# Optimization experiments

Measured on AMD Instinct MI355X. Metric: run time of the kernel, lower is better.

Reference implementation:

```python
import jax, jax.numpy as jnp
import numpy as np

S, B, H, L = 256, 256, 1024, 3  # seq_len, batch, hidden(=input), num_layers


def setup_inputs() -> dict:
    key = jax.random.key(0)
    k1, k2, k3 = jax.random.split(key, 3)
    scale = 1.0 / np.sqrt(H)
    return {
        "x": jax.random.normal(k1, (S, B, H), dtype=jnp.float32),
        "h_0": jnp.zeros((L, B, H), dtype=jnp.float32),
        "W_ih": jax.random.normal(k2, (L, H, H), dtype=jnp.float32) * scale,
        "W_hh": jax.random.normal(k3, (L, H, H), dtype=jnp.float32) * scale,
        "b_ih": jnp.zeros((L, H), dtype=jnp.float32),
        "b_hh": jnp.zeros((L, H), dtype=jnp.float32),
    }


def reference(x, h_0, W_ih, W_hh, b_ih, b_hh):
    L_ = W_ih.shape[0]

    def step(h_prev, x_t):
        # h_prev: [L, B, H], x_t: [B, H]
        inp = x_t
        hs = []
        for l in range(L_):
            h_l = jnp.tanh(inp @ W_ih[l].T + b_ih[l] + h_prev[l] @ W_hh[l].T + b_hh[l])
            hs.append(h_l)
            inp = h_l
        h_next = jnp.stack(hs, axis=0)
        return h_next, hs[-1]

    h_N, y = jax.lax.scan(step, h_0, x)
    return y, h_N
```

## Files before the change

### kernel.cpp

```cpp
#include <hip/hip_runtime.h>
#include <math.h>


#define S_LEN  256
#define BATCH  256
#define HID    1024
#define NLAY   3
#define RING   4
#define COLS   32
#define ROWS   128
#define GROUP  32
#define TOTAL_WG     192
#define THREADS      256

typedef _Float16 v8h __attribute__((ext_vector_type(8)));
typedef float    v4f __attribute__((ext_vector_type(4)));

#define MFMA16(a, b, c) __builtin_amdgcn_mfma_f32_16x16x32_f16((a), (b), (c), 0, 0, 0)

#define FLAG(l, t, rb) (((l) * S_LEN + (t)) * 2 + (rb))

__device__ __forceinline__ void spin_wait(int* p, int target) {
  while (__hip_atomic_load(p, __ATOMIC_RELAXED, __HIP_MEMORY_SCOPE_AGENT) < target) {
    __builtin_amdgcn_s_sleep(1);
  }
}

__global__ void rnn_pre(const float* __restrict__ x,
                        const float* __restrict__ h0,
                        _Float16* __restrict__ hring,
                        _Float16* __restrict__ x16,
                        int* __restrict__ done,
                        int convert_x) {
  const size_t idx = (size_t)blockIdx.x * blockDim.x + threadIdx.x;
  if (idx < NLAY * S_LEN * 2) done[idx] = 0;
  if (idx < (size_t)NLAY * BATCH * HID) {
    const int l   = (int)(idx / (BATCH * HID));
    const int off = (int)(idx - (size_t)l * (BATCH * HID));
    hring[(size_t)(l * RING + (RING - 1)) * BATCH * HID + off] = (_Float16)h0[idx];
  }
  if (convert_x) {
    const size_t base = idx * 8;
    if (base < (size_t)S_LEN * BATCH * HID) {
      v4f f0 = *(const v4f*)(x + base);
      v4f f1 = *(const v4f*)(x + base + 4);
      v8h v;
#pragma unroll
      for (int j = 0; j < 4; ++j) {
        v[j]     = (_Float16)f0[j];
        v[j + 4] = (_Float16)f1[j];
      }
      *(v8h*)(x16 + base) = v;
    }
  }
}

__global__ __launch_bounds__(THREADS, 1) void rnn_main(
    const float* __restrict__ x,
    const _Float16* __restrict__ x16,
    const float* __restrict__ W_ih, const float* __restrict__ W_hh,
    const float* __restrict__ b_ih, const float* __restrict__ b_hh,
    float* __restrict__ out,
    _Float16* __restrict__ hring, int* __restrict__ done) {
  __shared__ _Float16 WB[64][2][64][8];

  const int tid  = threadIdx.x;
  const int lane = tid & 63;
  const int wave = tid >> 6;
  const int wg   = blockIdx.x;
  const int l    = wg >> 6;
  const int sub  = wg & 63;
  const int rb   = sub >> 5;
  const int cb   = sub & 31;

  for (int i = tid; i < 64 * 2 * 64; i += THREADS) {
    const int kc = i >> 7;
    const int ct = (i >> 6) & 1;
    const int ln = i & 63;
    const int c    = ct * 16 + (ln & 15);
    const int k0   = kc * 32 + ((ln >> 4) << 3);
    const int gcol = cb * COLS + c;
    const float* src = (k0 < HID)
        ? (W_ih + (size_t)l * HID * HID + (size_t)gcol * HID + k0)
        : (W_hh + (size_t)l * HID * HID + (size_t)gcol * HID + (k0 - HID));
    v8h w;
#pragma unroll
    for (int j = 0; j < 8; ++j) w[j] = (_Float16)src[j];
    *(v8h*)(&WB[kc][ct][ln][0]) = w;
  }

  const int   c0    = cb * COLS + (lane & 15);
  const float bias0 = b_ih[l * HID + c0]      + b_hh[l * HID + c0];
  const float bias1 = b_ih[l * HID + c0 + 16] + b_hh[l * HID + c0 + 16];
  __syncthreads();

  const int rowbase = rb * ROWS + wave * 32;
  const int r0      = rowbase + (lane & 15);
  const int kfrag   = (lane >> 4) << 3;

  for (int t = 0; t < S_LEN; ++t) {
    v4f acc[2][2];
#pragma unroll
    for (int a = 0; a < 2; ++a)
#pragma unroll
      for (int b = 0; b < 2; ++b) acc[a][b] = (v4f){0.f, 0.f, 0.f, 0.f};

    if (l == 0) {
      if (x16) {
        const _Float16* a0p = x16 + (size_t)t * BATCH * HID + (size_t)r0 * HID + kfrag;
        const _Float16* a1p = a0p + (size_t)16 * HID;
#pragma unroll 8
        for (int kc = 0; kc < 32; ++kc) {
          v8h a0 = *(const v8h*)(a0p + kc * 32);
          v8h a1 = *(const v8h*)(a1p + kc * 32);
          v8h b0 = *(const v8h*)(&WB[kc][0][lane][0]);
          v8h b1 = *(const v8h*)(&WB[kc][1][lane][0]);
          acc[0][0] = MFMA16(a0, b0, acc[0][0]);
          acc[0][1] = MFMA16(a0, b1, acc[0][1]);
          acc[1][0] = MFMA16(a1, b0, acc[1][0]);
          acc[1][1] = MFMA16(a1, b1, acc[1][1]);
        }
      } else {
        const float* a0p = x + (size_t)t * BATCH * HID + (size_t)r0 * HID + kfrag;
        const float* a1p = a0p + (size_t)16 * HID;
#pragma unroll 4
        for (int kc = 0; kc < 32; ++kc) {
          v4f f0 = *(const v4f*)(a0p + kc * 32);
          v4f f1 = *(const v4f*)(a0p + kc * 32 + 4);
          v4f g0 = *(const v4f*)(a1p + kc * 32);
          v4f g1 = *(const v4f*)(a1p + kc * 32 + 4);
          v8h a0, a1;
#pragma unroll
          for (int j = 0; j < 4; ++j) {
            a0[j]     = (_Float16)f0[j];
            a0[j + 4] = (_Float16)f1[j];
            a1[j]     = (_Float16)g0[j];
            a1[j + 4] = (_Float16)g1[j];
          }
          v8h b0 = *(const v8h*)(&WB[kc][0][lane][0]);
          v8h b1 = *(const v8h*)(&WB[kc][1][lane][0]);
          acc[0][0] = MFMA16(a0, b0, acc[0][0]);
          acc[0][1] = MFMA16(a0, b1, acc[0][1]);
          acc[1][0] = MFMA16(a1, b0, acc[1][0]);
          acc[1][1] = MFMA16(a1, b1, acc[1][1]);
        }
      }
    }

    if (tid == 0) {
      if (t > 0)                      spin_wait(&done[FLAG(l, t - 1, rb)], GROUP);
      if (l < NLAY - 1 && t >= RING)  spin_wait(&done[FLAG(l + 1, t - RING, rb)], GROUP);
    }
    __syncthreads();
    __builtin_amdgcn_fence(__ATOMIC_ACQUIRE, "agent");

    {
      const _Float16* base = hring + (size_t)(l * RING + ((t + RING - 1) & (RING - 1))) * BATCH * HID;
      const _Float16* a0p  = base + (size_t)r0 * HID + kfrag;
      const _Float16* a1p  = a0p + (size_t)16 * HID;
#pragma unroll 8
      for (int kc = 0; kc < 32; ++kc) {
        v8h a0 = *(const v8h*)(a0p + kc * 32);
        v8h a1 = *(const v8h*)(a1p + kc * 32);
        v8h b0 = *(const v8h*)(&WB[kc + 32][0][lane][0]);
        v8h b1 = *(const v8h*)(&WB[kc + 32][1][lane][0]);
        acc[0][0] = MFMA16(a0, b0, acc[0][0]);
        acc[0][1] = MFMA16(a0, b1, acc[0][1]);
        acc[1][0] = MFMA16(a1, b0, acc[1][0]);
        acc[1][1] = MFMA16(a1, b1, acc[1][1]);
      }
    }

    if (l > 0) {
      if (tid == 0) spin_wait(&done[FLAG(l - 1, t, rb)], GROUP);
      __syncthreads();
      __builtin_amdgcn_fence(__ATOMIC_ACQUIRE, "agent");

      const _Float16* base = hring + (size_t)((l - 1) * RING + (t & (RING - 1))) * BATCH * HID;
      const _Float16* a0p  = base + (size_t)r0 * HID + kfrag;
      const _Float16* a1p  = a0p + (size_t)16 * HID;
#pragma unroll 8
      for (int kc = 0; kc < 32; ++kc) {
        v8h a0 = *(const v8h*)(a0p + kc * 32);
        v8h a1 = *(const v8h*)(a1p + kc * 32);
        v8h b0 = *(const v8h*)(&WB[kc][0][lane][0]);
        v8h b1 = *(const v8h*)(&WB[kc][1][lane][0]);
        acc[0][0] = MFMA16(a0, b0, acc[0][0]);
        acc[0][1] = MFMA16(a0, b1, acc[0][1]);
        acc[1][0] = MFMA16(a1, b0, acc[1][0]);
        acc[1][1] = MFMA16(a1, b1, acc[1][1]);
      }
    }

    _Float16* hout = hring + (size_t)(l * RING + (t & (RING - 1))) * BATCH * HID;
    float*    yout = out + (size_t)t * BATCH * HID;
    float*    hN   = out + (size_t)S_LEN * BATCH * HID + (size_t)l * BATCH * HID;
    const int qrow = (lane >> 4) << 2;
    const int ccol = lane & 15;
#pragma unroll
    for (int rt = 0; rt < 2; ++rt) {
#pragma unroll
      for (int ct = 0; ct < 2; ++ct) {
        const float bb   = (ct == 0) ? bias0 : bias1;
        const int   colg = cb * COLS + ct * 16 + ccol;
#pragma unroll
        for (int i = 0; i < 4; ++i) {
          const int rowg = rowbase + rt * 16 + qrow + i;
          const float hv = tanhf(acc[rt][ct][i] + bb);
          hout[(size_t)rowg * HID + colg] = (_Float16)hv;
          if (l == NLAY - 1)  yout[(size_t)rowg * HID + colg] = hv;
          if (t == S_LEN - 1) hN[(size_t)rowg * HID + colg]   = hv;
        }
      }
    }

    __syncthreads();
    if (tid == 0) {
      __hip_atomic_fetch_add(&done[FLAG(l, t, rb)], 1, __ATOMIC_RELEASE, __HIP_MEMORY_SCOPE_AGENT);
    }
  }
}

extern "C" void kernel_launch(void* const* d_in, const int* in_sizes, int n_in,
                              void* d_out, int out_size, void* d_ws, size_t ws_size,
                              hipStream_t stream) {
  (void)in_sizes; (void)n_in; (void)out_size;
  const float* x    = (const float*)d_in[0];
  const float* h0   = (const float*)d_in[1];
  const float* W_ih = (const float*)d_in[2];
  const float* W_hh = (const float*)d_in[3];
  const float* b_ih = (const float*)d_in[4];
  const float* b_hh = (const float*)d_in[5];
  float* out = (float*)d_out;

  int*      done  = (int*)d_ws;
  _Float16* hring = (_Float16*)((char*)d_ws + 8192);

  const size_t ring_bytes = (size_t)NLAY * RING * BATCH * HID * sizeof(_Float16);
  const size_t x16_off    = 8192 + ring_bytes;
  const size_t x16_bytes  = (size_t)S_LEN * BATCH * HID * sizeof(_Float16);
  const int    use_x16    = (ws_size >= x16_off + x16_bytes) ? 1 : 0;
  _Float16*    x16        = use_x16 ? (_Float16*)((char*)d_ws + x16_off) : (_Float16*)0;

  const int pre_elems  = use_x16 ? (S_LEN * BATCH * HID / 8) : (NLAY * BATCH * HID);
  const int pre_blocks = (pre_elems + THREADS - 1) / THREADS;
  rnn_pre<<<pre_blocks, THREADS, 0, stream>>>(x, h0, hring, x16, done, use_x16);
  rnn_main<<<TOTAL_WG, THREADS, 0, stream>>>(x, x16, W_ih, W_hh, b_ih, b_hh, out, hring, done);
}
```

Baseline: 8.737 ms.

## Use per-wave spin waits, 8 waves per block, deeper ring, fast tanh

```diff
diff --git a/kernel.cpp b/kernel.cpp
--- a/kernel.cpp
+++ b/kernel.cpp
@@ -6,12 +6,12 @@
 #define BATCH  256
 #define HID    1024
 #define NLAY   3
-#define RING   4
+#define RING   8
 #define COLS   32
 #define ROWS   128
 #define GROUP  32
 #define TOTAL_WG     192
-#define THREADS      256
+#define THREADS      512
 
 typedef _Float16 v8h __attribute__((ext_vector_type(8)));
 typedef float    v4f __attribute__((ext_vector_type(4)));
@@ -20,10 +20,15 @@
 
 #define FLAG(l, t, rb) (((l) * S_LEN + (t)) * 2 + (rb))
 
-__device__ __forceinline__ void spin_wait(int* p, int target) {
+__device__ __forceinline__ void wave_wait(int* p, int target) {
   while (__hip_atomic_load(p, __ATOMIC_RELAXED, __HIP_MEMORY_SCOPE_AGENT) < target) {
     __builtin_amdgcn_s_sleep(1);
   }
+}
+
+__device__ __forceinline__ float tanh_fast(float x) {
+  const float e = __expf(2.0f * x);
+  return 1.0f - 2.0f * __builtin_amdgcn_rcpf(e + 1.0f);
 }
 
 __global__ void rnn_pre(const float* __restrict__ x,
@@ -94,101 +99,75 @@
   const float bias1 = b_ih[l * HID + c0 + 16] + b_hh[l * HID + c0 + 16];
   __syncthreads();
 
-  const int rowbase = rb * ROWS + wave * 32;
+  const int rowbase = rb * ROWS + wave * 16;
   const int r0      = rowbase + (lane & 15);
   const int kfrag   = (lane >> 4) << 3;
 
   for (int t = 0; t < S_LEN; ++t) {
-    v4f acc[2][2];
-#pragma unroll
-    for (int a = 0; a < 2; ++a)
-#pragma unroll
-      for (int b = 0; b < 2; ++b) acc[a][b] = (v4f){0.f, 0.f, 0.f, 0.f};
+    v4f acc[2];
+    acc[0] = (v4f){0.f, 0.f, 0.f, 0.f};
+    acc[1] = (v4f){0.f, 0.f, 0.f, 0.f};
 
     if (l == 0) {
       if (x16) {
-        const _Float16* a0p = x16 + (size_t)t * BATCH * HID + (size_t)r0 * HID + kfrag;
-        const _Float16* a1p = a0p + (size_t)16 * HID;
+        const _Float16* ap = x16 + (size_t)t * BATCH * HID + (size_t)r0 * HID + kfrag;
 #pragma unroll 8
         for (int kc = 0; kc < 32; ++kc) {
-          v8h a0 = *(const v8h*)(a0p + kc * 32);
-          v8h a1 = *(const v8h*)(a1p + kc * 32);
+          v8h a  = *(const v8h*)(ap + kc * 32);
           v8h b0 = *(const v8h*)(&WB[kc][0][lane][0]);
           v8h b1 = *(const v8h*)(&WB[kc][1][lane][0]);
-          acc[0][0] = MFMA16(a0, b0, acc[0][0]);
-          acc[0][1] = MFMA16(a0, b1, acc[0][1]);
-          acc[1][0] = MFMA16(a1, b0, acc[1][0]);
-          acc[1][1] = MFMA16(a1, b1, acc[1][1]);
+          acc[0] = MFMA16(a, b0, acc[0]);
+          acc[1] = MFMA16(a, b1, acc[1]);
         }
       } else {
-        const float* a0p = x + (size_t)t * BATCH * HID + (size_t)r0 * HID + kfrag;
-        const float* a1p = a0p + (size_t)16 * HID;
+        const float* ap = x + (size_t)t * BATCH * HID + (size_t)r0 * HID + kfrag;
 #pragma unroll 4
         for (int kc = 0; kc < 32; ++kc) {
-          v4f f0 = *(const v4f*)(a0p + kc * 32);
-          v4f f1 = *(const v4f*)(a0p + kc * 32 + 4);
-          v4f g0 = *(const v4f*)(a1p + kc * 32);
-          v4f g1 = *(const v4f*)(a1p + kc * 32 + 4);
-          v8h a0, a1;
+          v4f f0 = *(const v4f*)(ap + kc * 32);
+          v4f f1 = *(const v4f*)(ap + kc * 32 + 4);
+          v8h a;
 #pragma unroll
           for (int j = 0; j < 4; ++j) {
-            a0[j]     = (_Float16)f0[j];
-            a0[j + 4] = (_Float16)f1[j];
-            a1[j]     = (_Float16)g0[j];
-            a1[j + 4] = (_Float16)g1[j];
+            a[j]     = (_Float16)f0[j];
+            a[j + 4] = (_Float16)f1[j];
           }
           v8h b0 = *(const v8h*)(&WB[kc][0][lane][0]);
           v8h b1 = *(const v8h*)(&WB[kc][1][lane][0]);
-          acc[0][0] = MFMA16(a0, b0, acc[0][0]);
-          acc[0][1] = MFMA16(a0, b1, acc[0][1]);
-          acc[1][0] = MFMA16(a1, b0, acc[1][0]);
-          acc[1][1] = MFMA16(a1, b1, acc[1][1]);
+          acc[0] = MFMA16(a, b0, acc[0]);
+          acc[1] = MFMA16(a, b1, acc[1]);
         }
       }
-    }
-
-    if (tid == 0) {
-      if (t > 0)                      spin_wait(&done[FLAG(l, t - 1, rb)], GROUP);
-      if (l < NLAY - 1 && t >= RING)  spin_wait(&done[FLAG(l + 1, t - RING, rb)], GROUP);
-    }
-    __syncthreads();
-    __builtin_amdgcn_fence(__ATOMIC_ACQUIRE, "agent");
-
-    {
-      const _Float16* base = hring + (size_t)(l * RING + ((t + RING - 1) & (RING - 1))) * BATCH * HID;
-      const _Float16* a0p  = base + (size_t)r0 * HID + kfrag;
-      const _Float16* a1p  = a0p + (size_t)16 * HID;
+    } else {
+      wave_wait(&done[FLAG(l - 1, t, rb)], GROUP);
+      __builtin_amdgcn_fence(__ATOMIC_ACQUIRE, "agent");
+      const _Float16* ap = hring
+          + (size_t)((l - 1) * RING + (t & (RING - 1))) * BATCH * HID
+          + (size_t)r0 * HID + kfrag;
 #pragma unroll 8
       for (int kc = 0; kc < 32; ++kc) {
-        v8h a0 = *(const v8h*)(a0p + kc * 32);
-        v8h a1 = *(const v8h*)(a1p + kc * 32);
+        v8h a  = *(const v8h*)(ap + kc * 32);
+        v8h b0 = *(const v8h*)(&WB[kc][0][lane][0]);
+        v8h b1 = *(const v8h*)(&WB[kc][1][lane][0]);
+        acc[0] = MFMA16(a, b0, acc[0]);
+        acc[1] = MFMA16(a, b1, acc[1]);
+      }
+    }
+
+    if (t > 0)                      wave_wait(&done[FLAG(l, t - 1, rb)], GROUP);
+    if (l < NLAY - 1 && t >= RING)  wave_wait(&done[FLAG(l + 1, t - RING, rb)], GROUP);
+    __builtin_amdgcn_fence(__ATOMIC_ACQUIRE, "agent");
+
+    {
+      const _Float16* ap = hring
+          + (size_t)(l * RING + ((t + RING - 1) & (RING - 1))) * BATCH * HID
+          + (size_t)r0 * HID + kfrag;
+#pragma unroll 8
+      for (int kc = 0; kc < 32; ++kc) {
+        v8h a  = *(const v8h*)(ap + kc * 32);
         v8h b0 = *(const v8h*)(&WB[kc + 32][0][lane][0]);
         v8h b1 = *(const v8h*)(&WB[kc + 32][1][lane][0]);
-        acc[0][0] = MFMA16(a0, b0, acc[0][0]);
-        acc[0][1] = MFMA16(a0, b1, acc[0][1]);
-        acc[1][0] = MFMA16(a1, b0, acc[1][0]);
-        acc[1][1] = MFMA16(a1, b1, acc[1][1]);
-      }
-    }
-
-    if (l > 0) {
-      if (tid == 0) spin_wait(&done[FLAG(l - 1, t, rb)], GROUP);
-      __syncthreads();
-      __builtin_amdgcn_fence(__ATOMIC_ACQUIRE, "agent");
-
-      const _Float16* base = hring + (size_t)((l - 1) * RING + (t & (RING - 1))) * BATCH * HID;
-      const _Float16* a0p  = base + (size_t)r0 * HID + kfrag;
-      const _Float16* a1p  = a0p + (size_t)16 * HID;
-#pragma unroll 8
-      for (int kc = 0; kc < 32; ++kc) {
-        v8h a0 = *(const v8h*)(a0p + kc * 32);
-        v8h a1 = *(const v8h*)(a1p + kc * 32);
-        v8h b0 = *(const v8h*)(&WB[kc][0][lane][0]);
-        v8h b1 = *(const v8h*)(&WB[kc][1][lane][0]);
-        acc[0][0] = MFMA16(a0, b0, acc[0][0]);
-        acc[0][1] = MFMA16(a0, b1, acc[0][1]);
-        acc[1][0] = MFMA16(a1, b0, acc[1][0]);
-        acc[1][1] = MFMA16(a1, b1, acc[1][1]);
+        acc[0] = MFMA16(a, b0, acc[0]);
+        acc[1] = MFMA16(a, b1, acc[1]);
       }
     }
 
@@ -198,19 +177,16 @@
     const int qrow = (lane >> 4) << 2;
     const int ccol = lane & 15;
 #pragma unroll
-    for (int rt = 0; rt < 2; ++rt) {
-#pragma unroll
-      for (int ct = 0; ct < 2; ++ct) {
-        const float bb   = (ct == 0) ? bias0 : bias1;
-        const int   colg = cb * COLS + ct * 16 + ccol;
-#pragma unroll
-        for (int i = 0; i < 4; ++i) {
-          const int rowg = rowbase + rt * 16 + qrow + i;
-          const float hv = tanhf(acc[rt][ct][i] + bb);
-          hout[(size_t)rowg * HID + colg] = (_Float16)hv;
-          if (l == NLAY - 1)  yout[(size_t)rowg * HID + colg] = hv;
-          if (t == S_LEN - 1) hN[(size_t)rowg * HID + colg]   = hv;
-        }
+    for (int ct = 0; ct < 2; ++ct) {
+      const float bb   = (ct == 0) ? bias0 : bias1;
+      const int   colg = cb * COLS + ct * 16 + ccol;
+#pragma unroll
+      for (int i = 0; i < 4; ++i) {
+        const int rowg = rowbase + qrow + i;
+        const float hv = tanh_fast(acc[ct][i] + bb);
+        hout[(size_t)rowg * HID + colg] = (_Float16)hv;
+        if (l == NLAY - 1)  yout[(size_t)rowg * HID + colg] = hv;
+        if (t == S_LEN - 1) hN[(size_t)rowg * HID + colg]   = hv;
       }
     }
 
@@ -242,8 +218,10 @@
   const int    use_x16    = (ws_size >= x16_off + x16_bytes) ? 1 : 0;
   _Float16*    x16        = use_x16 ? (_Float16*)((char*)d_ws + x16_off) : (_Float16*)0;
 
-  const int pre_elems  = use_x16 ? (S_LEN * BATCH * HID / 8) : (NLAY * BATCH * HID);
-  const int pre_blocks = (pre_elems + THREADS - 1) / THREADS;
-  rnn_pre<<<pre_blocks, THREADS, 0, stream>>>(x, h0, hring, x16, done, use_x16);
+  const int pre_threads = 256;
+  const size_t pre_elems = use_x16 ? ((size_t)S_LEN * BATCH * HID / 8)
+                                   : ((size_t)NLAY * BATCH * HID);
+  const int pre_blocks = (int)((pre_elems + pre_threads - 1) / pre_threads);
+  rnn_pre<<<pre_blocks, pre_threads, 0, stream>>>(x, h0, hring, x16, done, use_x16);
   rnn_main<<<TOTAL_WG, THREADS, 0, stream>>>(x, x16, W_ih, W_hh, b_ih, b_hh, out, hring, done);
 }
```

Measured after the change: 8.445 ms. -3.3%, faster.
